# Kernel tuning notes

Measured on AMD Instinct MI355X. Metric: run time of the kernel, lower is better.

## Reference

```python
import jax, jax.numpy as jnp
import numpy as np
from jax import lax

B, H, W, CIN, COUT, K, SDIM = 8, 256, 256, 128, 128, 3, 512


def setup_inputs() -> dict:
    key = jax.random.key(0)
    k1, k2, k3, k4, k5 = jax.random.split(key, 5)
    return {
        "x": jax.random.normal(k1, (B, H, W, CIN), dtype=jnp.float32),
        "style": jax.random.normal(k2, (B, SDIM), dtype=jnp.float32),
        "kernel": jax.random.normal(k3, (K, K, CIN, COUT), dtype=jnp.float32),
        "w_mod": jax.random.normal(k4, (SDIM, CIN), dtype=jnp.float32) / np.sqrt(SDIM),
        "b_mod": jnp.zeros((CIN,), dtype=jnp.float32),
        "noise_strength": jnp.zeros((1,), dtype=jnp.float32),
        "bias": jnp.zeros((COUT,), dtype=jnp.float32),
        "noise": jax.random.normal(k5, (B, H, W, 1), dtype=jnp.float32),
    }


def reference(x, style, kernel, w_mod, b_mod, noise_strength, bias, noise):
    kh, kw, cin, cout = kernel.shape
    # equalized-lr runtime coefficient
    he_std = 1.0 / jnp.sqrt(jnp.asarray(kh * kw * cin, jnp.float32))
    w = kernel * he_std  # [kh,kw,cin,cout]
    # style modulation (Dense with zero constant bias) + 1
    s = style @ w_mod + b_mod + 1.0  # [B, cin]
    # demodulate=True: normalize by global max-abs of style (as in source)
    s = s * (1.0 / jnp.max(jnp.abs(s)))
    # NOTE: source uses style[0] only -> single shared modulated weight
    w = w * s[0][None, None, :, None]
    d = lax.rsqrt(jnp.sum(jnp.square(w), axis=(0, 1, 2)) + 1e-8)  # [cout]
    w = w * d[None, None, None, :]
    # plain conv branch: NHWC, stride 1, SAME padding
    y = lax.conv_general_dilated(
        x, w, window_strides=(1, 1), padding="SAME",
        dimension_numbers=("NHWC", "HWIO", "NHWC"))
    # noise injection (noise_strength is zero-init, kept for faithfulness)
    y = y + noise * (noise_strength / 2.0)
    y = y + bias
    # lrelu(0.2) * sqrt(2)
    y = jnp.where(y >= 0, y, 0.2 * y) * jnp.sqrt(jnp.asarray(2.0, y.dtype))
    return y
```

## Files before the change

### kernel.cpp

```cpp
#include <hip/hip_runtime.h>
#include <hip/hip_bf16.h>

#define H 256
#define W 256
#define CIN 128
#define COUT 128
#define BATCH 8
#define LDA 136

typedef float f32x4 __attribute__((ext_vector_type(4)));
typedef short bf16x8 __attribute__((ext_vector_type(8)));

static __device__ __forceinline__ unsigned short f2bf(float f) {
    unsigned int x = __float_as_uint(f);
    unsigned int r = (x + 0x7fffu + ((x >> 16) & 1u)) >> 16;
    return (unsigned short)r;
}

__device__ float g_s0[CIN];
__device__ float g_bmax[BATCH];
__device__ float g_partial[9 * COUT];

__global__ __launch_bounds__(256) void mod_style(
    const float* __restrict__ style, const float* __restrict__ w_mod,
    const float* __restrict__ b_mod)
{
    __shared__ float red[256];
    const int t = threadIdx.x;
    const int b = blockIdx.x;
    const int c = t & 127;
    const int half = t >> 7;

    float acc = 0.f;
    const float4* st4 = (const float4*)(style + b * 512 + half * 256);
    const float* wm = w_mod + half * 256 * CIN + c;
    for (int k4 = 0; k4 < 64; ++k4) {
        float4 s4 = st4[k4];
        const float* w = wm + k4 * 4 * CIN;
        acc += s4.x * w[0 * CIN];
        acc += s4.y * w[1 * CIN];
        acc += s4.z * w[2 * CIN];
        acc += s4.w * w[3 * CIN];
    }
    red[t] = acc;
    __syncthreads();
    if (t < 128) {
        float sval = red[t] + red[t + 128] + b_mod[t] + 1.0f;
        if (b == 0) g_s0[t] = sval;
        red[t] = fabsf(sval);
    }
    __syncthreads();
    for (int off = 64; off > 0; off >>= 1) {
        if (t < off) red[t] = fmaxf(red[t], red[t + off]);
        __syncthreads();
    }
    if (t == 0) g_bmax[b] = red[0];
}

__global__ __launch_bounds__(256) void demod_partial(
    const float* __restrict__ kern)
{
    __shared__ float scale[CIN];
    __shared__ float red[256];
    const int t = threadIdx.x;
    const int kk = blockIdx.x;
    const int co = t & 127;
    const int half = t >> 7;

    if (t < 128) {
        float m = g_bmax[0];
        #pragma unroll
        for (int i = 1; i < BATCH; ++i) m = fmaxf(m, g_bmax[i]);
        const float he_std = 1.0f / sqrtf(1152.0f);
        scale[t] = g_s0[t] * (1.0f / m) * he_std;
    }
    __syncthreads();

    float ss = 0.f;
    const float* kbase = kern + (size_t)kk * 128 * 128 + co;
    for (int j = 0; j < 64; ++j) {
        int ci = half * 64 + j;
        float wv = kbase[(size_t)ci * 128] * scale[ci];
        ss += wv * wv;
    }
    red[t] = ss;
    __syncthreads();
    if (t < 128) g_partial[kk * 128 + t] = red[t] + red[t + 128];
}

__global__ __launch_bounds__(256) void swizzle_kernel(
    const float* __restrict__ kern, unsigned short* __restrict__ wprep)
{
    __shared__ float scale[CIN];
    __shared__ float dArr[COUT];
    const int t = threadIdx.x;
    const int u = blockIdx.x * 256 + t;

    if (t < 128) {
        float m = g_bmax[0];
        #pragma unroll
        for (int i = 1; i < BATCH; ++i) m = fmaxf(m, g_bmax[i]);
        const float he_std = 1.0f / sqrtf(1152.0f);
        scale[t] = g_s0[t] * (1.0f / m) * he_std;
        float sum = 0.f;
        #pragma unroll
        for (int g = 0; g < 9; ++g) sum += g_partial[g * 128 + t];
        dArr[t] = rsqrtf(sum + 1e-8f);
    }
    __syncthreads();

    const int lane  = u & 63;
    const int ntile = (u >> 6) & 7;
    const int kc    = (u >> 9) & 3;
    const int kk    = u >> 11;
    const int co  = ntile * 16 + (lane & 15);
    const int cib = kc * 32 + (lane >> 4) * 8;
    const float dv = dArr[co];
    unsigned int packed[4];
    #pragma unroll
    for (int jp = 0; jp < 4; ++jp) {
        int ci0 = cib + jp * 2;
        float w0 = kern[(kk * 128 + ci0)     * 128 + co] * scale[ci0]     * dv;
        float w1 = kern[(kk * 128 + ci0 + 1) * 128 + co] * scale[ci0 + 1] * dv;
        packed[jp] = (unsigned int)f2bf(w0) | ((unsigned int)f2bf(w1) << 16);
    }
    ((uint4*)wprep)[u] = make_uint4(packed[0], packed[1], packed[2], packed[3]);
}

__global__ __launch_bounds__(256, 3) void conv_kernel(
    const float* __restrict__ x, const unsigned short* __restrict__ wprep,
    const float* __restrict__ noise_strength, const float* __restrict__ bias,
    const float* __restrict__ noise, float* __restrict__ out)
{
    __shared__ unsigned short ldsA[130 * LDA];
    const int tid  = threadIdx.x;
    const int lane = tid & 63;
    const int wave = tid >> 6;
    const int wm = wave & 1;
    const int wn = wave >> 1;
    const int wt = blockIdx.x;
    const int h  = blockIdx.y;
    const int b  = blockIdx.z;
    const int wstart = wt * 128;

    f32x4 acc[4][4];
    const f32x4 zero = {0.f, 0.f, 0.f, 0.f};
    for (int i = 0; i < 4; ++i)
        for (int j = 0; j < 4; ++j) acc[i][j] = zero;

    const bf16x8* bb = (const bf16x8*)wprep + wn * 256 + lane;
    bf16x8 bcur[4];
    #pragma unroll
    for (int j = 0; j < 4; ++j) bcur[j] = bb[j * 64];

    for (int kh = 0; kh < 3; ++kh) {
        __syncthreads();
        const int hImg = h + kh - 1;
        const bool rowValid = (hImg >= 0) && (hImg < H);
        const float* rowPtr = x + ((size_t)(b * H + hImg) * W) * CIN;
        for (int idx = tid; idx < 130 * 32; idx += 256) {
            int p  = idx >> 5;
            int c4 = idx & 31;
            int wImg = wstart - 1 + p;
            float4 v = make_float4(0.f, 0.f, 0.f, 0.f);
            if (rowValid && (unsigned)wImg < (unsigned)W)
                v = *(const float4*)(rowPtr + (size_t)wImg * CIN + c4 * 4);
            ushort4 u;
            u.x = f2bf(v.x); u.y = f2bf(v.y); u.z = f2bf(v.z); u.w = f2bf(v.w);
            *(ushort4*)&ldsA[p * LDA + c4 * 4] = u;
        }
        __syncthreads();

        #pragma unroll
        for (int kw = 0; kw < 3; ++kw) {
            #pragma unroll
            for (int kc = 0; kc < 4; ++kc) {
                const int p12 = kw * 4 + kc;
                int gn;
                if (p12 == 11) gn = (kh == 2) ? 0 : (kh + 1) * 12;
                else           gn = kh * 12 + p12 + 1;
                bf16x8 bnxt[4];
                #pragma unroll
                for (int j = 0; j < 4; ++j) bnxt[j] = bb[gn * 512 + j * 64];

                const int ka = kc * 32 + (lane >> 4) * 8;
                #pragma unroll
                for (int i = 0; i < 4; ++i) {
                    int m = wm * 64 + i * 16 + (lane & 15) + kw;
                    bf16x8 af = *(const bf16x8*)&ldsA[m * LDA + ka];
                    #pragma unroll
                    for (int j = 0; j < 4; ++j)
                        acc[i][j] = __builtin_amdgcn_mfma_f32_16x16x32_bf16(
                            af, bcur[j], acc[i][j], 0, 0, 0);
                }
                #pragma unroll
                for (int j = 0; j < 4; ++j) bcur[j] = bnxt[j];
            }
        }
    }

    const float ns  = noise_strength[0] * 0.5f;
    const float RT2 = 1.41421356237309515f;
    const size_t pixBase = ((size_t)(b * H + h) * W) + wstart;
    #pragma unroll
    for (int i = 0; i < 4; ++i) {
        const int mbase = wm * 64 + i * 16 + ((lane >> 4) << 2);
        #pragma unroll
        for (int r = 0; r < 4; ++r) {
            const size_t pix = pixBase + (mbase + r);
            const float nz = noise[pix] * ns;
            #pragma unroll
            for (int j = 0; j < 4; ++j) {
                const int col = wn * 64 + j * 16 + (lane & 15);
                float v = acc[i][j][r] + nz + bias[col];
                v = (v >= 0.f ? v : 0.2f * v) * RT2;
                out[pix * COUT + col] = v;
            }
        }
    }
}

extern "C" void kernel_launch(void* const* d_in, const int* in_sizes, int n_in,
                              void* d_out, int out_size, void* d_ws, size_t ws_size,
                              hipStream_t stream) {
    const float* x              = (const float*)d_in[0];
    const float* style          = (const float*)d_in[1];
    const float* kern           = (const float*)d_in[2];
    const float* w_mod          = (const float*)d_in[3];
    const float* b_mod          = (const float*)d_in[4];
    const float* noise_strength = (const float*)d_in[5];
    const float* bias           = (const float*)d_in[6];
    const float* noise          = (const float*)d_in[7];
    float* out = (float*)d_out;
    unsigned short* wprep = (unsigned short*)d_ws;

    hipLaunchKernelGGL(mod_style, dim3(8), dim3(256), 0, stream,
                       style, w_mod, b_mod);
    hipLaunchKernelGGL(demod_partial, dim3(9), dim3(256), 0, stream, kern);
    hipLaunchKernelGGL(swizzle_kernel, dim3(72), dim3(256), 0, stream,
                       kern, wprep);
    hipLaunchKernelGGL(conv_kernel, dim3(2, 256, 8), dim3(256), 0, stream,
                       x, wprep, noise_strength, bias, noise, out);
}
```

Measured before the change: 601.7 us.

## Stream 16 output rows per block with a 4-slot rolling LDS row buffer

The conv kernel now has each 128-thread block process a 64-pixel-wide strip over 16 consecutive output rows. It keeps a ring of 4 bf16 input rows in LDS so each input row is loaded and converted once rather than three times. Loading of the next row is split into two register-staged halves that are interleaved with the MFMA work for the current row, and noise loads are hoisted ahead of the last kh pass. The grid shrinks from 4096 to 512 blocks of 2 waves each. This cuts redundant global reads and conversions, but lowers parallelism and raises register pressure from the staging buffers.

After: 868.5 us. 44.3% more time.

```diff
diff --git a/kernel.cpp b/kernel.cpp
--- a/kernel.cpp
+++ b/kernel.cpp
@@ -7,6 +7,7 @@
 #define COUT 128
 #define BATCH 8
 #define LDA 136
+#define SLOT (66 * LDA)
 
 typedef float f32x4 __attribute__((ext_vector_type(4)));
 typedef short bf16x8 __attribute__((ext_vector_type(8)));
@@ -127,94 +128,180 @@
     ((uint4*)wprep)[u] = make_uint4(packed[0], packed[1], packed[2], packed[3]);
 }
 
-__global__ __launch_bounds__(256, 3) void conv_kernel(
+template<int KH>
+static __device__ __forceinline__ void compute_kh(
+    const unsigned short* __restrict__ slot,
+    const bf16x8* __restrict__ bb,
+    bf16x8 (&bcur)[4], f32x4 (&acc)[4][4], const int lane)
+{
+    #pragma unroll
+    for (int kw = 0; kw < 3; ++kw) {
+        #pragma unroll
+        for (int kc = 0; kc < 4; ++kc) {
+            const int g = KH * 12 + kw * 4 + kc;
+            const int gn = (g == 35) ? 0 : g + 1;
+            bf16x8 bnxt[4];
+            #pragma unroll
+            for (int j = 0; j < 4; ++j) bnxt[j] = bb[gn * 512 + j * 64];
+            const int ka = kc * 32 + (lane >> 4) * 8;
+            #pragma unroll
+            for (int i = 0; i < 4; ++i) {
+                const int m = i * 16 + (lane & 15) + kw;
+                bf16x8 af = *(const bf16x8*)&slot[m * LDA + ka];
+                #pragma unroll
+                for (int j = 0; j < 4; ++j)
+                    acc[i][j] = __builtin_amdgcn_mfma_f32_16x16x32_bf16(
+                        af, bcur[j], acc[i][j], 0, 0, 0);
+            }
+            #pragma unroll
+            for (int j = 0; j < 4; ++j) bcur[j] = bnxt[j];
+        }
+    }
+}
+
+__global__ __launch_bounds__(128) void conv_kernel(
     const float* __restrict__ x, const unsigned short* __restrict__ wprep,
     const float* __restrict__ noise_strength, const float* __restrict__ bias,
     const float* __restrict__ noise, float* __restrict__ out)
 {
-    __shared__ unsigned short ldsA[130 * LDA];
+    __shared__ unsigned short ldsA[4 * SLOT];
     const int tid  = threadIdx.x;
     const int lane = tid & 63;
-    const int wave = tid >> 6;
-    const int wm = wave & 1;
-    const int wn = wave >> 1;
+    const int wn   = tid >> 6;
     const int wt = blockIdx.x;
-    const int h  = blockIdx.y;
+    const int hs = blockIdx.y * 16;
     const int b  = blockIdx.z;
-    const int wstart = wt * 128;
-
-    f32x4 acc[4][4];
-    const f32x4 zero = {0.f, 0.f, 0.f, 0.f};
-    for (int i = 0; i < 4; ++i)
-        for (int j = 0; j < 4; ++j) acc[i][j] = zero;
+    const int wstart = wt * 64;
+
+    #pragma unroll 1
+    for (int pr = 0; pr < 3; ++pr) {
+        const int ri = hs + pr - 1;
+        const bool rv = ((unsigned)ri < (unsigned)H);
+        const float* rp = x + ((size_t)(b * H + ri) * W) * CIN;
+        unsigned short* sl = &ldsA[pr * SLOT];
+        #pragma unroll 1
+        for (int idx = tid; idx < 66 * 32; idx += 128) {
+            const int p  = idx >> 5;
+            const int c4 = idx & 31;
+            const int wImg = wstart - 1 + p;
+            float4 v = make_float4(0.f, 0.f, 0.f, 0.f);
+            if (rv && (unsigned)wImg < (unsigned)W)
+                v = *(const float4*)(rp + (size_t)wImg * CIN + c4 * 4);
+            ushort4 u;
+            u.x = f2bf(v.x); u.y = f2bf(v.y); u.z = f2bf(v.z); u.w = f2bf(v.w);
+            *(ushort4*)&sl[p * LDA + c4 * 4] = u;
+        }
+    }
 
     const bf16x8* bb = (const bf16x8*)wprep + wn * 256 + lane;
     bf16x8 bcur[4];
     #pragma unroll
     for (int j = 0; j < 4; ++j) bcur[j] = bb[j * 64];
 
-    for (int kh = 0; kh < 3; ++kh) {
-        __syncthreads();
-        const int hImg = h + kh - 1;
-        const bool rowValid = (hImg >= 0) && (hImg < H);
-        const float* rowPtr = x + ((size_t)(b * H + hImg) * W) * CIN;
-        for (int idx = tid; idx < 130 * 32; idx += 256) {
-            int p  = idx >> 5;
-            int c4 = idx & 31;
-            int wImg = wstart - 1 + p;
-            float4 v = make_float4(0.f, 0.f, 0.f, 0.f);
-            if (rowValid && (unsigned)wImg < (unsigned)W)
-                v = *(const float4*)(rowPtr + (size_t)wImg * CIN + c4 * 4);
-            ushort4 u;
-            u.x = f2bf(v.x); u.y = f2bf(v.y); u.z = f2bf(v.z); u.w = f2bf(v.w);
-            *(ushort4*)&ldsA[p * LDA + c4 * 4] = u;
-        }
-        __syncthreads();
-
-        #pragma unroll
-        for (int kw = 0; kw < 3; ++kw) {
-            #pragma unroll
-            for (int kc = 0; kc < 4; ++kc) {
-                const int p12 = kw * 4 + kc;
-                int gn;
-                if (p12 == 11) gn = (kh == 2) ? 0 : (kh + 1) * 12;
-                else           gn = kh * 12 + p12 + 1;
-                bf16x8 bnxt[4];
-                #pragma unroll
-                for (int j = 0; j < 4; ++j) bnxt[j] = bb[gn * 512 + j * 64];
-
-                const int ka = kc * 32 + (lane >> 4) * 8;
-                #pragma unroll
-                for (int i = 0; i < 4; ++i) {
-                    int m = wm * 64 + i * 16 + (lane & 15) + kw;
-                    bf16x8 af = *(const bf16x8*)&ldsA[m * LDA + ka];
-                    #pragma unroll
-                    for (int j = 0; j < 4; ++j)
-                        acc[i][j] = __builtin_amdgcn_mfma_f32_16x16x32_bf16(
-                            af, bcur[j], acc[i][j], 0, 0, 0);
-                }
-                #pragma unroll
-                for (int j = 0; j < 4; ++j) bcur[j] = bnxt[j];
-            }
-        }
-    }
-
     const float ns  = noise_strength[0] * 0.5f;
     const float RT2 = 1.41421356237309515f;
-    const size_t pixBase = ((size_t)(b * H + h) * W) + wstart;
+    float bfl[4];
     #pragma unroll
-    for (int i = 0; i < 4; ++i) {
-        const int mbase = wm * 64 + i * 16 + ((lane >> 4) << 2);
-        #pragma unroll
-        for (int r = 0; r < 4; ++r) {
-            const size_t pix = pixBase + (mbase + r);
-            const float nz = noise[pix] * ns;
-            #pragma unroll
-            for (int j = 0; j < 4; ++j) {
-                const int col = wn * 64 + j * 16 + (lane & 15);
-                float v = acc[i][j][r] + nz + bias[col];
-                v = (v >= 0.f ? v : 0.2f * v) * RT2;
-                out[pix * COUT + col] = v;
+    for (int j = 0; j < 4; ++j) bfl[j] = bias[wn * 64 + j * 16 + (lane & 15)];
+
+    f32x4 acc[4][4];
+
+    #pragma unroll 1
+    for (int r = 0; r < 16; ++r) {
+        __syncthreads();
+
+        #pragma unroll
+        for (int i = 0; i < 4; ++i)
+            #pragma unroll
+            for (int j = 0; j < 4; ++j)
+                acc[i][j] = (f32x4){0.f, 0.f, 0.f, 0.f};
+
+        const bool doStage = (r < 15);
+        const int riA = hs + r + 2;
+        const bool rvA = ((unsigned)riA < (unsigned)H);
+        const float* rpA = x + ((size_t)(b * H + riA) * W) * CIN;
+
+        float4 stA[9];
+        if (doStage) {
+            #pragma unroll
+            for (int k = 0; k < 9; ++k) {
+                const int idx = tid + k * 128;
+                const int p = idx >> 5, c4 = idx & 31;
+                const int wImg = wstart - 1 + p;
+                stA[k] = make_float4(0.f, 0.f, 0.f, 0.f);
+                if (rvA && (unsigned)wImg < (unsigned)W)
+                    stA[k] = *(const float4*)(rpA + (size_t)wImg * CIN + c4 * 4);
+            }
+        }
+
+        compute_kh<0>(&ldsA[((r + 0) & 3) * SLOT], bb, bcur, acc, lane);
+
+        unsigned short* sw = &ldsA[((r + 3) & 3) * SLOT];
+        if (doStage) {
+            #pragma unroll
+            for (int k = 0; k < 9; ++k) {
+                const int idx = tid + k * 128;
+                const int p = idx >> 5, c4 = idx & 31;
+                ushort4 u;
+                u.x = f2bf(stA[k].x); u.y = f2bf(stA[k].y);
+                u.z = f2bf(stA[k].z); u.w = f2bf(stA[k].w);
+                *(ushort4*)&sw[p * LDA + c4 * 4] = u;
+            }
+        }
+
+        float4 stB[8];
+        if (doStage) {
+            #pragma unroll
+            for (int k = 0; k < 8; ++k) {
+                const int idx = 1152 + tid + k * 128;
+                const int p = idx >> 5, c4 = idx & 31;
+                const int wImg = wstart - 1 + p;
+                stB[k] = make_float4(0.f, 0.f, 0.f, 0.f);
+                if (idx < 2112 && rvA && (unsigned)wImg < (unsigned)W)
+                    stB[k] = *(const float4*)(rpA + (size_t)wImg * CIN + c4 * 4);
+            }
+        }
+
+        compute_kh<1>(&ldsA[((r + 1) & 3) * SLOT], bb, bcur, acc, lane);
+
+        if (doStage) {
+            #pragma unroll
+            for (int k = 0; k < 8; ++k) {
+                const int idx = 1152 + tid + k * 128;
+                if (idx < 2112) {
+                    const int p = idx >> 5, c4 = idx & 31;
+                    ushort4 u;
+                    u.x = f2bf(stB[k].x); u.y = f2bf(stB[k].y);
+                    u.z = f2bf(stB[k].z); u.w = f2bf(stB[k].w);
+                    *(ushort4*)&sw[p * LDA + c4 * 4] = u;
+                }
+            }
+        }
+
+        const int hrow = hs + r;
+        const size_t pixBase = ((size_t)(b * H + hrow) * W) + wstart;
+        float nz[4][4];
+        #pragma unroll
+        for (int i = 0; i < 4; ++i)
+            #pragma unroll
+            for (int rr = 0; rr < 4; ++rr)
+                nz[i][rr] = noise[pixBase + i * 16 + ((lane >> 4) << 2) + rr] * ns;
+
+        compute_kh<2>(&ldsA[((r + 2) & 3) * SLOT], bb, bcur, acc, lane);
+
+        #pragma unroll
+        for (int i = 0; i < 4; ++i) {
+            const int mbase = i * 16 + ((lane >> 4) << 2);
+            #pragma unroll
+            for (int rr = 0; rr < 4; ++rr) {
+                const size_t pix = pixBase + (mbase + rr);
+                #pragma unroll
+                for (int j = 0; j < 4; ++j) {
+                    const int col = wn * 64 + j * 16 + (lane & 15);
+                    float v = acc[i][j][rr] + nz[i][rr] + bfl[j];
+                    v = (v >= 0.f ? v : 0.2f * v) * RT2;
+                    out[pix * COUT + col] = v;
+                }
             }
         }
     }
@@ -239,6 +326,6 @@
     hipLaunchKernelGGL(demod_partial, dim3(9), dim3(256), 0, stream, kern);
     hipLaunchKernelGGL(swizzle_kernel, dim3(72), dim3(256), 0, stream,
                        kern, wprep);
-    hipLaunchKernelGGL(conv_kernel, dim3(2, 256, 8), dim3(256), 0, stream,
+    hipLaunchKernelGGL(conv_kernel, dim3(4, 16, 8), dim3(128), 0, stream,
                        x, wprep, noise_strength, bias, noise, out);
 }
```
